# Kernel optimization log

Measured on AMD Instinct MI355X. Metric: run time of the kernel, lower is better.

## Reference

```python
import jax, jax.numpy as jnp
import numpy as np

B, N, G = 8, 512, 16          # images, proposals/img, gt boxes/img
C = 91                        # num classes (incl background)
FEAT = 256 * 7 * 7            # pooled RoI feature dim = 12544
REP = 1024                    # TwoMLPHead representation size
FG, BG = 0.5, 0.5             # fg/bg IoU thresholds
BBOX_W = (10.0, 10.0, 5.0, 5.0)
BETA = 1.0 / 9.0              # smooth-L1 beta


def setup_inputs() -> dict:
    key = jax.random.key(0)
    ks = jax.random.split(key, 12)
    # valid xyxy boxes inside an ~800x800 image
    tl = jax.random.uniform(ks[0], (B, N, 2), minval=0.0, maxval=700.0)
    wh = jax.random.uniform(ks[1], (B, N, 2), minval=8.0, maxval=128.0)
    proposals = jnp.concatenate([tl, tl + wh], axis=-1)
    gtl = jax.random.uniform(ks[2], (B, G, 2), minval=0.0, maxval=700.0)
    gwh = jax.random.uniform(ks[3], (B, G, 2), minval=8.0, maxval=128.0)
    gt_boxes = jnp.concatenate([gtl, gtl + gwh], axis=-1)
    gt_labels = jax.random.randint(ks[4], (B, G), 1, C)  # foreground labels 1..C-1
    P = N + G
    features = jax.random.normal(ks[5], (B * P, FEAT), dtype=jnp.float32)
    s = 0.01
    return {
        'proposals': proposals, 'gt_boxes': gt_boxes, 'features': features,
        'W1': jax.random.normal(ks[6], (FEAT, REP), jnp.float32) * s,
        'b1': jnp.zeros((REP,), jnp.float32),
        'W2': jax.random.normal(ks[7], (REP, REP), jnp.float32) * s,
        'b2': jnp.zeros((REP,), jnp.float32),
        'Wcls': jax.random.normal(ks[8], (REP, C), jnp.float32) * s,
        'bcls': jnp.zeros((C,), jnp.float32),
        'Wbox': jax.random.normal(ks[9], (REP, C * 4), jnp.float32) * s,
        'bbox': jnp.zeros((C * 4,), jnp.float32),
        'gt_labels': gt_labels,
    }


def _box_iou(gt, pr):
    # gt: [B,G,4], pr: [B,P,4] -> [B,G,P]
    area_g = (gt[..., 2] - gt[..., 0]) * (gt[..., 3] - gt[..., 1])
    area_p = (pr[..., 2] - pr[..., 0]) * (pr[..., 3] - pr[..., 1])
    lt = jnp.maximum(gt[:, :, None, :2], pr[:, None, :, :2])
    rb = jnp.minimum(gt[:, :, None, 2:], pr[:, None, :, 2:])
    wh = jnp.clip(rb - lt, 0.0)
    inter = wh[..., 0] * wh[..., 1]
    return inter / (area_g[:, :, None] + area_p[:, None, :] - inter)


def _encode(ref, gt):
    # torchvision BoxCoder.encode_single; ref/gt: [...,4]
    wx, wy, ww, wh = BBOX_W
    ew = ref[..., 2] - ref[..., 0]; eh = ref[..., 3] - ref[..., 1]
    ex = ref[..., 0] + 0.5 * ew;    ey = ref[..., 1] + 0.5 * eh
    gw = gt[..., 2] - gt[..., 0];   gh = gt[..., 3] - gt[..., 1]
    gx = gt[..., 0] + 0.5 * gw;     gy = gt[..., 1] + 0.5 * gh
    return jnp.stack([
        wx * (gx - ex) / ew, wy * (gy - ey) / eh,
        ww * jnp.log(gw / ew), wh * jnp.log(gh / eh)], axis=-1)


def reference(proposals, gt_boxes, features, W1, b1, W2, b2, Wcls, bcls, Wbox, bbox, gt_labels):
    # add_gt_proposals
    props = jnp.concatenate([proposals, gt_boxes], axis=1)  # [B,P,4]
    # assign_targets_to_proposals (Matcher, allow_low_quality_matches=False)
    iou = _box_iou(gt_boxes, props)                          # [B,G,P]
    matched_vals = iou.max(axis=1)                           # [B,P]
    matched_idx = iou.argmax(axis=1)                         # [B,P]
    labels = jnp.take_along_axis(gt_labels, matched_idx, axis=1)
    labels = jnp.where(matched_vals < BG, 0, labels)                         # background
    labels = jnp.where((matched_vals >= BG) & (matched_vals < FG), -1, labels)  # ignore
    matched_gt = jnp.take_along_axis(gt_boxes, matched_idx[..., None], axis=1)  # [B,P,4]
    reg_targets = _encode(props, matched_gt).reshape(-1, 4)  # [R,4]
    labels = labels.reshape(-1)                               # [R]

    # TwoMLPHead + FastRCNNPredictor
    x = jax.nn.relu(features @ W1 + b1)
    x = jax.nn.relu(x @ W2 + b2)
    class_logits = x @ Wcls + bcls                            # [R,C]
    box_regression = (x @ Wbox + bbox).reshape(-1, C, 4)      # [R,C,4]

    # fastrcnn_loss (all proposals; ignored labels (-1) masked from CE)
    R = class_logits.shape[0]
    valid = (labels >= 0).astype(class_logits.dtype)
    safe_lab = jnp.clip(labels, 0, C - 1)
    logp = jax.nn.log_softmax(class_logits, axis=-1)
    nll = -jnp.take_along_axis(logp, safe_lab[:, None], axis=1)[:, 0]
    classification_loss = (nll * valid).sum() / jnp.maximum(valid.sum(), 1.0)

    pos = (labels > 0).astype(class_logits.dtype)
    pred = jnp.take_along_axis(box_regression, safe_lab[:, None, None], axis=1)[:, 0]  # [R,4]
    d = jnp.abs(pred - reg_targets)
    sl1 = jnp.where(d < BETA, 0.5 * d * d / BETA, d - 0.5 * BETA).sum(-1)
    box_loss = (sl1 * pos).sum() / R

    return jnp.stack([classification_loss, box_loss])
```

## Files before the change

kernel.cpp:

```cpp
#include <hip/hip_runtime.h>
#include <cstdint>
#include <cstddef>

#define BQ   8
#define NP   512
#define GQ   16
#define PP   528
#define RT   4224
#define CC   91
#define FEATD 12544
#define REPD 1024
#define NH   512
#define NHU  455
#define BETA (1.0f/9.0f)
#define WSC  64.0f

typedef float f32x4 __attribute__((ext_vector_type(4)));
typedef int   v8i  __attribute__((ext_vector_type(8)));
typedef float v16f __attribute__((ext_vector_type(16)));

__device__ __forceinline__ unsigned short f2bf(float f) {
  unsigned int x = __float_as_uint(f);
  unsigned int r = (x + 0x7fffu + ((x >> 16) & 1u)) >> 16;
  return (unsigned short)r;
}
__device__ __forceinline__ float bf2f(unsigned short u) {
  return __uint_as_float((unsigned int)u << 16);
}

__device__ __forceinline__ void ld_lds16(const void* g, void* l) {
  __builtin_amdgcn_global_load_lds(
      (const __attribute__((address_space(1))) void*)g,
      (__attribute__((address_space(3))) void*)l, 16, 0, 0);
}

__device__ __forceinline__ size_t img_off(int row, int kb, int KT) {
  return (size_t)((row >> 7) * KT + (kb >> 6)) * 8192
       + (size_t)((((row >> 5) & 3) << 11) + (((kb >> 4) & 3) << 9)
                  + ((row & 31) << 4) + (kb & 15));
}

constexpr size_t O_W1T = 0;
constexpr size_t SZ_W1T = (size_t)FEATD * REPD;
constexpr size_t O_W2T = O_W1T + SZ_W1T;
constexpr size_t SZ_W2T = (size_t)REPD * REPD;
constexpr size_t O_WH  = O_W2T + SZ_W2T;
constexpr size_t SZ_WH = (size_t)NH * REPD;
constexpr size_t O_BH  = O_WH + SZ_WH;
constexpr size_t SZ_BH = (size_t)NH * 4;
constexpr size_t O_X1  = O_BH + SZ_BH;
constexpr size_t SZ_X1 = (size_t)RT * REPD;
constexpr size_t O_X2  = O_X1 + SZ_X1;
constexpr size_t O_LAB = O_X2 + SZ_X1;
constexpr size_t O_TGT = O_LAB + (size_t)RT * 4;
constexpr size_t O_NLL = O_TGT + (size_t)RT * 16;
constexpr size_t O_VC  = O_NLL + (size_t)RT * 4;
constexpr size_t O_SL1 = O_VC + (size_t)RT * 4;
constexpr size_t O_PART = ((O_SL1 + (size_t)RT * 4) + 255) & ~(size_t)255;
constexpr size_t SZ_PART = (size_t)4 * RT * REPD * 2;
constexpr size_t O_F8 = O_PART + SZ_PART;

#define NB_CV ((RT/128)*(FEATD/64))
__global__ void prep_cv(const float* __restrict__ feat, unsigned char* __restrict__ feat8) {
  int b = blockIdx.x, t = threadIdx.x;
  int yb = b / (FEATD / 64), kt = b % (FEATD / 64);
  const int w = t >> 6, L = t & 63;
  const int rl = L & 31, h = L >> 5;
  const float* src = feat + (size_t)(yb * 128 + w * 32 + rl) * FEATD + kt * 64 + h * 32;
  unsigned char* dst = feat8 + (size_t)b * 8192 + w * 2048 + rl * 16;
  unsigned int pk[8];
#pragma unroll
  for (int c = 0; c < 8; ++c) {
    float4 f = ((const float4*)src)[c];
    unsigned int r = (unsigned int)__builtin_amdgcn_cvt_pk_fp8_f32(f.x, f.y, 0, false);
    pk[c] = (unsigned int)__builtin_amdgcn_cvt_pk_fp8_f32(f.z, f.w, (int)r, true);
  }
  int4 v0; v0.x = (int)pk[0]; v0.y = (int)pk[1]; v0.z = (int)pk[2]; v0.w = (int)pk[3];
  int4 v1; v1.x = (int)pk[4]; v1.y = (int)pk[5]; v1.z = (int)pk[6]; v1.w = (int)pk[7];
  *(int4*)(dst + (2 * h) * 512) = v0;
  *(int4*)(dst + (2 * h + 1) * 512) = v1;
}

__device__ __forceinline__ void tr128(const float* __restrict__ in, unsigned char* __restrict__ out,
                                      int K, int N, int row_off, int KT,
                                      int bx, int by, int t, float (*tile)[36]) {
  const int n0 = bx * 32, k0 = by * 128;
  const int n4 = t & 7, kr = t >> 3;
  if (n0 + 32 <= N) {
#pragma unroll
    for (int i = 0; i < 4; ++i) {
      int k = k0 + kr + i * 32;
      float4 f = *(const float4*)&in[(size_t)k * N + n0 + n4 * 4];
      *(float4*)&tile[kr + i * 32][n4 * 4] = f;
    }
  } else {
#pragma unroll
    for (int i = 0; i < 4; ++i) {
      int k = k0 + kr + i * 32;
#pragma unroll
      for (int j = 0; j < 4; ++j) {
        int n = n0 + n4 * 4 + j;
        tile[kr + i * 32][n4 * 4 + j] = (n < N) ? in[(size_t)k * N + n] : 0.0f;
      }
    }
  }
  __syncthreads();
  const int rn = t & 31, kc = t >> 5;
  const int n = n0 + rn;
  if (n < N) {
    unsigned int pk[4];
#pragma unroll
    for (int q = 0; q < 4; ++q) {
      float f0 = tile[kc * 16 + q * 4 + 0][rn] * WSC;
      float f1 = tile[kc * 16 + q * 4 + 1][rn] * WSC;
      float f2 = tile[kc * 16 + q * 4 + 2][rn] * WSC;
      float f3 = tile[kc * 16 + q * 4 + 3][rn] * WSC;
      unsigned int r = (unsigned int)__builtin_amdgcn_cvt_pk_fp8_f32(f0, f1, 0, false);
      pk[q] = (unsigned int)__builtin_amdgcn_cvt_pk_fp8_f32(f2, f3, (int)r, true);
    }
    int4 v; v.x = (int)pk[0]; v.y = (int)pk[1]; v.z = (int)pk[2]; v.w = (int)pk[3];
    *(int4*)&out[img_off(n + row_off, k0 + kc * 16, KT)] = v;
  }
}

#define NBW1 ((REPD/32)*(FEATD/128))
#define NBW2 ((REPD/32)*(REPD/128))
#define NBWC (3*(REPD/128))
#define NBWB (12*(REPD/128))
#define NB_PW (NBW1+NBW2+NBWC+NBWB)

__global__ void prep_w(const float* __restrict__ W1, const float* __restrict__ W2,
                       const float* __restrict__ Wcls, const float* __restrict__ Wbox,
                       unsigned char* __restrict__ W1t, unsigned char* __restrict__ W2t,
                       unsigned char* __restrict__ Wh) {
  __shared__ float tile[128][36];
  int b = blockIdx.x, t = threadIdx.x;
  if (b < NBW1) { tr128(W1, W1t, FEATD, REPD, 0, FEATD/64, b % 32, b / 32, t, tile); return; }
  b -= NBW1;
  if (b < NBW2) { tr128(W2, W2t, REPD, REPD, 0, REPD/64, b % 32, b / 32, t, tile); return; }
  b -= NBW2;
  if (b < NBWC) { tr128(Wcls, Wh, REPD, CC, 0, REPD/64, b % 3, b / 3, t, tile); return; }
  b -= NBWC;
  tr128(Wbox, Wh, REPD, 4 * CC, CC, REPD/64, b % 12, b / 12, t, tile);
}

#define NB_HI 230
#define NB_MT 17
#define NB_MISC (NB_HI+NB_MT)
__global__ void prep_misc(const float* __restrict__ bcls, const float* __restrict__ bbox,
                          const float* __restrict__ proposals, const float* __restrict__ gt_boxes,
                          const int* __restrict__ gt_labels,
                          unsigned char* __restrict__ Wh, float* __restrict__ bh,
                          int* __restrict__ labels, float* __restrict__ tgts) {
  int b = blockIdx.x, t = threadIdx.x;
  if (b < NB_HI) {
    int idx = b * 256 + t;
    const int npad = (NH - NHU) * REPD;
    if (idx < npad) {
      int row = NHU + (idx >> 10), k = idx & 1023;
      Wh[img_off(row, k, REPD/64)] = 0;
    } else {
      int i2 = idx - npad;
      if (i2 < NH) bh[i2] = (i2 < CC) ? bcls[i2] : (i2 < NHU ? bbox[i2 - CC] : 0.0f);
    }
    return;
  }
  b -= NB_HI;
  int r = b * 256 + t;
  if (r >= RT) return;
  int bi_ = r / PP, p = r % PP;
  float x0, y0, x1, y1;
  if (p < NP) {
    const float* qq = proposals + ((size_t)bi_ * NP + p) * 4;
    x0 = qq[0]; y0 = qq[1]; x1 = qq[2]; y1 = qq[3];
  } else {
    const float* qq = gt_boxes + ((size_t)bi_ * GQ + (p - NP)) * 4;
    x0 = qq[0]; y0 = qq[1]; x1 = qq[2]; y1 = qq[3];
  }
  float ap = (x1 - x0) * (y1 - y0);
  float best = -1.0f; int bg = 0;
#pragma unroll
  for (int g = 0; g < GQ; ++g) {
    const float* gb = gt_boxes + ((size_t)bi_ * GQ + g) * 4;
    float gx0 = gb[0], gy0 = gb[1], gx1 = gb[2], gy1 = gb[3];
    float ag = (gx1 - gx0) * (gy1 - gy0);
    float iw = fmaxf(fminf(gx1, x1) - fmaxf(gx0, x0), 0.0f);
    float ih = fmaxf(fminf(gy1, y1) - fmaxf(gy0, y0), 0.0f);
    float inter = iw * ih;
    float iou = inter / (ag + ap - inter);
    if (iou > best) { best = iou; bg = g; }
  }
  int lab = gt_labels[bi_ * GQ + bg];
  if (best < 0.5f) lab = 0;
  labels[r] = lab;
  const float* gb = gt_boxes + ((size_t)bi_ * GQ + bg) * 4;
  float ew = x1 - x0, eh = y1 - y0;
  float ex = x0 + 0.5f * ew, ey = y0 + 0.5f * eh;
  float gw = gb[2] - gb[0], gh = gb[3] - gb[1];
  float gx = gb[0] + 0.5f * gw, gy = gb[1] + 0.5f * gh;
  tgts[r * 4 + 0] = 10.0f * (gx - ex) / ew;
  tgts[r * 4 + 1] = 10.0f * (gy - ey) / eh;
  tgts[r * 4 + 2] = 5.0f * logf(gw / ew);
  tgts[r * 4 + 3] = 5.0f * logf(gh / eh);
}

__global__ __launch_bounds__(256, 4)
void gemm_f8(const unsigned char* __restrict__ Aimg, const unsigned char* __restrict__ Bimg,
             unsigned short* __restrict__ P, int M, int Nc, int KT, int nkt,
             int n_nblk, int n_my, int npairs) {
  __shared__ unsigned char As[2 * 8192];
  __shared__ unsigned char Bs[2 * 8192];

  const int g = blockIdx.x;
  const int xcd = g & 7;
  const int kix = g >> 3;
  const int n  = kix % n_nblk;
  const int pi = kix / n_nblk;
  const int p  = pi * 8 + xcd;
  if (p >= npairs) return;
  const int y  = p % n_my;
  const int kz = p / n_my;
  const int m0 = y * 128, n0 = n * 128;

  const int tid = threadIdx.x;
  const int w = tid >> 6, L = tid & 63;
  const int l31 = L & 31, h = L >> 5;
  const int wr = (w >> 1) * 64, wc = (w & 1) * 64;

  const int kt0 = kz * nkt;
  const unsigned char* gA = Aimg + ((size_t)y * KT + kt0) * 8192 + w * 2048 + L * 16;
  const unsigned char* gB = Bimg + ((size_t)n * KT + kt0) * 8192 + w * 2048 + L * 16;
  const int lw = w * 2048;

#define STAGE(it, bufo) do {                                    \
    const size_t _go = (size_t)(it) * 8192;                     \
    ld_lds16(gA + _go,        &As[(bufo) + lw]);                \
    ld_lds16(gA + _go + 1024, &As[(bufo) + lw + 1024]);         \
    ld_lds16(gB + _go,        &Bs[(bufo) + lw]);                \
    ld_lds16(gB + _go + 1024, &Bs[(bufo) + lw + 1024]);         \
  } while (0)

  int aoff[2], boff[2];
#pragma unroll
  for (int i = 0; i < 2; ++i) {
    aoff[i] = (((w >> 1) * 2 + i) << 11) + (h << 10) + (l31 << 4);
    boff[i] = (((w & 1) * 2 + i) << 11) + (h << 10) + (l31 << 4);
  }

  STAGE(0, 0);

  v16f acc[2][2] = {};
  int cur = 0;
  for (int it = 0; it < nkt; ++it) {
    const int cb = cur << 13;
    if (it + 1 < nkt) {
      STAGE(it + 1, cb ^ 8192);
      asm volatile("s_waitcnt vmcnt(4)" ::: "memory");
    } else {
      asm volatile("s_waitcnt vmcnt(0)" ::: "memory");
    }
    __builtin_amdgcn_sched_barrier(0);
    __builtin_amdgcn_s_barrier();

    v8i a[2], b[2];
#pragma unroll
    for (int i = 0; i < 2; ++i) {
      int4 alo = *(const int4*)&As[cb + aoff[i]];
      int4 ahi = *(const int4*)&As[cb + aoff[i] + 512];
      a[i] = (v8i){alo.x, alo.y, alo.z, alo.w, ahi.x, ahi.y, ahi.z, ahi.w};
      int4 blo = *(const int4*)&Bs[cb + boff[i]];
      int4 bhi = *(const int4*)&Bs[cb + boff[i] + 512];
      b[i] = (v8i){blo.x, blo.y, blo.z, blo.w, bhi.x, bhi.y, bhi.z, bhi.w};
    }
#pragma unroll
    for (int i = 0; i < 2; ++i)
#pragma unroll
      for (int j = 0; j < 2; ++j)
        acc[i][j] = __builtin_amdgcn_mfma_scale_f32_32x32x64_f8f6f4(
            a[i], b[j], acc[i][j], 0, 0, 0, 127, 0, 127);

    asm volatile("s_waitcnt lgkmcnt(0)" ::: "memory");
    __builtin_amdgcn_sched_barrier(0);
    __builtin_amdgcn_s_barrier();
    cur ^= 1;
  }
#undef STAGE

  unsigned short* Pz = P + (size_t)kz * M * Nc;
#pragma unroll
  for (int i = 0; i < 2; ++i) {
#pragma unroll
    for (int j = 0; j < 2; ++j) {
      int colb = n0 + wc + j * 32 + l31;
#pragma unroll
      for (int r = 0; r < 16; ++r) {
        int row = m0 + wr + i * 32 + (r & 3) + 8 * (r >> 2) + 4 * h;
        Pz[(size_t)row * Nc + colb] = f2bf(acc[i][j][r]);
      }
    }
  }
}

template <int S>
__global__ void reduce_fp8k(const unsigned short* __restrict__ P, const float* __restrict__ bias,
                            unsigned int* __restrict__ outp, long MN4, int nc4) {
  long i = (long)blockIdx.x * blockDim.x + threadIdx.x;
  long stride = (long)gridDim.x * blockDim.x;
  const ushort4* P4 = (const ushort4*)P;
  const float4* B4 = (const float4*)bias;
  for (; i < MN4; i += stride) {
    float vx = 0, vy = 0, vz = 0, vw = 0;
#pragma unroll
    for (int s = 0; s < S; ++s) {
      ushort4 u = P4[s * MN4 + i];
      vx += bf2f(u.x); vy += bf2f(u.y); vz += bf2f(u.z); vw += bf2f(u.w);
    }
    float4 b = B4[i & (nc4 - 1)];
    vx = fmaxf(vx * (1.0f / WSC) + b.x, 0.0f);
    vy = fmaxf(vy * (1.0f / WSC) + b.y, 0.0f);
    vz = fmaxf(vz * (1.0f / WSC) + b.z, 0.0f);
    vw = fmaxf(vw * (1.0f / WSC) + b.w, 0.0f);
    unsigned int r = (unsigned int)__builtin_amdgcn_cvt_pk_fp8_f32(vx, vy, 0, false);
    r = (unsigned int)__builtin_amdgcn_cvt_pk_fp8_f32(vz, vw, (int)r, true);
    int rr = (int)(i >> 8);
    int kb = ((int)i & 255) * 4;
    outp[img_off(rr, kb, REPD / 64) >> 2] = r;
  }
}

__global__ void loss_row(const unsigned short* __restrict__ P, const float* __restrict__ bh,
                         const int* __restrict__ labels, const float* __restrict__ tgts,
                         float* __restrict__ nll_v, float* __restrict__ vc_v,
                         float* __restrict__ sl1_v) {
  int r = blockIdx.x;
  int l = threadIdx.x;
  const size_t SL = (size_t)RT * NH;
  const unsigned short* p0 = P + (size_t)r * NH;
#define COLV(c) ((bf2f(p0[(c)]) + bf2f(p0[SL + (c)]) + bf2f(p0[2 * SL + (c)]) + \
                  bf2f(p0[3 * SL + (c)])) * (1.0f / WSC) + bh[(c)])
  float v1 = COLV(l);
  float v2 = (l < CC - 64) ? COLV(64 + l) : -3.4e38f;
  float m = fmaxf(v1, v2);
#pragma unroll
  for (int o = 32; o; o >>= 1) m = fmaxf(m, __shfl_xor(m, o));
  float e = __expf(v1 - m) + ((l < CC - 64) ? __expf(v2 - m) : 0.0f);
#pragma unroll
  for (int o = 32; o; o >>= 1) e += __shfl_xor(e, o);
  if (l == 0) {
    float lse = m + __logf(e);
    int lab = labels[r];
    int sl = lab < 0 ? 0 : (lab > CC - 1 ? CC - 1 : lab);
    float valid = (lab >= 0) ? 1.0f : 0.0f;
    nll_v[r] = (lse - COLV(sl)) * valid;
    vc_v[r] = valid;
    float s = 0.0f;
#pragma unroll
    for (int d = 0; d < 4; ++d) {
      float pd = COLV(CC + sl * 4 + d);
      float ad = fabsf(pd - tgts[r * 4 + d]);
      s += (ad < BETA) ? 0.5f * ad * ad / BETA : ad - 0.5f * BETA;
    }
    sl1_v[r] = (lab > 0) ? s : 0.0f;
  }
#undef COLV
}

__global__ void reduce_final(const float* __restrict__ nll_v, const float* __restrict__ vc_v,
                             const float* __restrict__ sl1_v, float* __restrict__ out) {
  __shared__ float s1[256], s2[256], s3[256];
  int t = threadIdx.x;
  float a = 0, b = 0, c = 0;
  for (int i = t; i < RT; i += 256) { a += nll_v[i]; b += vc_v[i]; c += sl1_v[i]; }
  s1[t] = a; s2[t] = b; s3[t] = c;
  __syncthreads();
  for (int o = 128; o; o >>= 1) {
    if (t < o) { s1[t] += s1[t + o]; s2[t] += s2[t + o]; s3[t] += s3[t + o]; }
    __syncthreads();
  }
  if (t == 0) {
    out[0] = s1[0] / fmaxf(s2[0], 1.0f);
    out[1] = s3[0] / (float)RT;
  }
}

extern "C" void kernel_launch(void* const* d_in, const int* in_sizes, int n_in,
                              void* d_out, int out_size, void* d_ws, size_t ws_size,
                              hipStream_t stream) {
  const float* proposals = (const float*)d_in[0];
  const float* gt_boxes  = (const float*)d_in[1];
  const float* features  = (const float*)d_in[2];
  const float* W1   = (const float*)d_in[3];
  const float* b1   = (const float*)d_in[4];
  const float* W2   = (const float*)d_in[5];
  const float* b2   = (const float*)d_in[6];
  const float* Wcls = (const float*)d_in[7];
  const float* bcls = (const float*)d_in[8];
  const float* Wbox = (const float*)d_in[9];
  const float* bbox = (const float*)d_in[10];
  const int* gt_labels = (const int*)d_in[11];
  float* out = (float*)d_out;

  char* ws = (char*)d_ws;
  unsigned char* W1t = (unsigned char*)(ws + O_W1T);
  unsigned char* W2t = (unsigned char*)(ws + O_W2T);
  unsigned char* Wh  = (unsigned char*)(ws + O_WH);
  float* bh          = (float*)(ws + O_BH);
  unsigned char* x1  = (unsigned char*)(ws + O_X1);
  unsigned char* x2  = (unsigned char*)(ws + O_X2);
  int* labels        = (int*)(ws + O_LAB);
  float* tgts        = (float*)(ws + O_TGT);
  float* nll_v       = (float*)(ws + O_NLL);
  float* vc_v        = (float*)(ws + O_VC);
  float* sl1_v       = (float*)(ws + O_SL1);
  unsigned short* part = (unsigned short*)(ws + O_PART);
  unsigned char* feat8 = (unsigned char*)(ws + O_F8);

  prep_cv<<<NB_CV, 256, 0, stream>>>(features, feat8);
  prep_w<<<NB_PW, 256, 0, stream>>>(W1, W2, Wcls, Wbox, W1t, W2t, Wh);
  prep_misc<<<NB_MISC, 256, 0, stream>>>(bcls, bbox, proposals, gt_boxes, gt_labels,
                                         Wh, bh, labels, tgts);

  gemm_f8<<<1088, 256, 0, stream>>>(feat8, W1t, part, RT, REPD, FEATD/64, 49,
                                    8, 33, 132);
  reduce_fp8k<4><<<2048, 256, 0, stream>>>(part, b1, (unsigned int*)x1,
                                           (long)RT * REPD / 4, REPD / 4);

  gemm_f8<<<576, 256, 0, stream>>>(x1, W2t, part, RT, REPD, REPD/64, 8,
                                   8, 33, 66);
  reduce_fp8k<2><<<2048, 256, 0, stream>>>(part, b2, (unsigned int*)x2,
                                           (long)RT * REPD / 4, REPD / 4);

  gemm_f8<<<544, 256, 0, stream>>>(x2, Wh, part, RT, NH, REPD/64, 4,
                                   4, 33, 132);

  loss_row<<<RT, 64, 0, stream>>>(part, bh, labels, tgts, nll_v, vc_v, sl1_v);
  reduce_final<<<1, 256, 0, stream>>>(nll_v, vc_v, sl1_v, out);
}
```

Measured before the change: 482.1 us.

## Enlarge FP8 GEMM tiles to 256x256 with 512-thread blocks and padded M

```diff
diff --git a/kernel.cpp b/kernel.cpp
--- a/kernel.cpp
+++ b/kernel.cpp
@@ -7,6 +7,7 @@
 #define GQ   16
 #define PP   528
 #define RT   4224
+#define MPAD 4352
 #define CC   91
 #define FEATD 12544
 #define REPD 1024
@@ -49,7 +50,7 @@
 constexpr size_t O_BH  = O_WH + SZ_WH;
 constexpr size_t SZ_BH = (size_t)NH * 4;
 constexpr size_t O_X1  = O_BH + SZ_BH;
-constexpr size_t SZ_X1 = (size_t)RT * REPD;
+constexpr size_t SZ_X1 = (size_t)MPAD * REPD;
 constexpr size_t O_X2  = O_X1 + SZ_X1;
 constexpr size_t O_LAB = O_X2 + SZ_X1;
 constexpr size_t O_TGT = O_LAB + (size_t)RT * 4;
@@ -57,17 +58,24 @@
 constexpr size_t O_VC  = O_NLL + (size_t)RT * 4;
 constexpr size_t O_SL1 = O_VC + (size_t)RT * 4;
 constexpr size_t O_PART = ((O_SL1 + (size_t)RT * 4) + 255) & ~(size_t)255;
-constexpr size_t SZ_PART = (size_t)4 * RT * REPD * 2;
+constexpr size_t SZ_PART = (size_t)4 * MPAD * REPD * 2;
 constexpr size_t O_F8 = O_PART + SZ_PART;
 
-#define NB_CV ((RT/128)*(FEATD/64))
+#define NKT1 (FEATD/64)
+#define NB_CV ((MPAD/128)*NKT1)
 __global__ void prep_cv(const float* __restrict__ feat, unsigned char* __restrict__ feat8) {
   int b = blockIdx.x, t = threadIdx.x;
-  int yb = b / (FEATD / 64), kt = b % (FEATD / 64);
+  int yb = b / NKT1, kt = b % NKT1;
   const int w = t >> 6, L = t & 63;
   const int rl = L & 31, h = L >> 5;
+  unsigned char* dst = feat8 + (size_t)b * 8192 + w * 2048 + rl * 16;
+  if (yb == 33) {
+    int4 z; z.x = z.y = z.z = z.w = 0;
+    *(int4*)(dst + (2 * h) * 512) = z;
+    *(int4*)(dst + (2 * h + 1) * 512) = z;
+    return;
+  }
   const float* src = feat + (size_t)(yb * 128 + w * 32 + rl) * FEATD + kt * 64 + h * 32;
-  unsigned char* dst = feat8 + (size_t)b * 8192 + w * 2048 + rl * 16;
   unsigned int pk[8];
 #pragma unroll
   for (int c = 0; c < 8; ++c) {
@@ -204,12 +212,12 @@
   tgts[r * 4 + 3] = 5.0f * logf(gh / eh);
 }
 
-__global__ __launch_bounds__(256, 4)
+__global__ __launch_bounds__(512, 4)
 void gemm_f8(const unsigned char* __restrict__ Aimg, const unsigned char* __restrict__ Bimg,
-             unsigned short* __restrict__ P, int M, int Nc, int KT, int nkt,
+             unsigned short* __restrict__ P, int Mp, int Nc, int KT, int nkt,
              int n_nblk, int n_my, int npairs) {
-  __shared__ unsigned char As[2 * 8192];
-  __shared__ unsigned char Bs[2 * 8192];
+  __shared__ unsigned char As[2 * 16384];
+  __shared__ unsigned char Bs[2 * 16384];
 
   const int g = blockIdx.x;
   const int xcd = g & 7;
@@ -220,16 +228,17 @@
   if (p >= npairs) return;
   const int y  = p % n_my;
   const int kz = p / n_my;
-  const int m0 = y * 128, n0 = n * 128;
+  const int m0 = y * 256, n0 = n * 256;
 
   const int tid = threadIdx.x;
   const int w = tid >> 6, L = tid & 63;
   const int l31 = L & 31, h = L >> 5;
-  const int wr = (w >> 1) * 64, wc = (w & 1) * 64;
 
   const int kt0 = kz * nkt;
-  const unsigned char* gA = Aimg + ((size_t)y * KT + kt0) * 8192 + w * 2048 + L * 16;
-  const unsigned char* gB = Bimg + ((size_t)n * KT + kt0) * 8192 + w * 2048 + L * 16;
+  const unsigned char* gA = Aimg + ((size_t)((2 * y + (w >> 2)) * KT + kt0)) * 8192
+                                 + (w & 3) * 2048 + L * 16;
+  const unsigned char* gB = Bimg + ((size_t)((2 * n + (w >> 2)) * KT + kt0)) * 8192
+                                 + (w & 3) * 2048 + L * 16;
   const int lw = w * 2048;
 
 #define STAGE(it, bufo) do {                                    \
@@ -240,21 +249,22 @@
     ld_lds16(gB + _go + 1024, &Bs[(bufo) + lw + 1024]);         \
   } while (0)
 
-  int aoff[2], boff[2];
-#pragma unroll
-  for (int i = 0; i < 2; ++i) {
-    aoff[i] = (((w >> 1) * 2 + i) << 11) + (h << 10) + (l31 << 4);
-    boff[i] = (((w & 1) * 2 + i) << 11) + (h << 10) + (l31 << 4);
-  }
+  int aoff[4], boff[2];
+#pragma unroll
+  for (int i = 0; i < 4; ++i)
+    aoff[i] = (((w >> 2) * 4 + i) << 11) + (h << 10) + (l31 << 4);
+#pragma unroll
+  for (int j = 0; j < 2; ++j)
+    boff[j] = (((w & 3) * 2 + j) << 11) + (h << 10) + (l31 << 4);
 
   STAGE(0, 0);
 
-  v16f acc[2][2] = {};
+  v16f acc[4][2] = {};
   int cur = 0;
   for (int it = 0; it < nkt; ++it) {
-    const int cb = cur << 13;
+    const int cb = cur << 14;
     if (it + 1 < nkt) {
-      STAGE(it + 1, cb ^ 8192);
+      STAGE(it + 1, cb ^ 16384);
       asm volatile("s_waitcnt vmcnt(4)" ::: "memory");
     } else {
       asm volatile("s_waitcnt vmcnt(0)" ::: "memory");
@@ -262,18 +272,21 @@
     __builtin_amdgcn_sched_barrier(0);
     __builtin_amdgcn_s_barrier();
 
-    v8i a[2], b[2];
-#pragma unroll
-    for (int i = 0; i < 2; ++i) {
+    v8i a[4], b[2];
+#pragma unroll
+    for (int i = 0; i < 4; ++i) {
       int4 alo = *(const int4*)&As[cb + aoff[i]];
       int4 ahi = *(const int4*)&As[cb + aoff[i] + 512];
       a[i] = (v8i){alo.x, alo.y, alo.z, alo.w, ahi.x, ahi.y, ahi.z, ahi.w};
-      int4 blo = *(const int4*)&Bs[cb + boff[i]];
-      int4 bhi = *(const int4*)&Bs[cb + boff[i] + 512];
-      b[i] = (v8i){blo.x, blo.y, blo.z, blo.w, bhi.x, bhi.y, bhi.z, bhi.w};
-    }
-#pragma unroll
-    for (int i = 0; i < 2; ++i)
+    }
+#pragma unroll
+    for (int j = 0; j < 2; ++j) {
+      int4 blo = *(const int4*)&Bs[cb + boff[j]];
+      int4 bhi = *(const int4*)&Bs[cb + boff[j] + 512];
+      b[j] = (v8i){blo.x, blo.y, blo.z, blo.w, bhi.x, bhi.y, bhi.z, bhi.w};
+    }
+#pragma unroll
+    for (int i = 0; i < 4; ++i)
 #pragma unroll
       for (int j = 0; j < 2; ++j)
         acc[i][j] = __builtin_amdgcn_mfma_scale_f32_32x32x64_f8f6f4(
@@ -286,15 +299,15 @@
   }
 #undef STAGE
 
-  unsigned short* Pz = P + (size_t)kz * M * Nc;
-#pragma unroll
-  for (int i = 0; i < 2; ++i) {
+  unsigned short* Pz = P + (size_t)kz * Mp * Nc;
+#pragma unroll
+  for (int i = 0; i < 4; ++i) {
 #pragma unroll
     for (int j = 0; j < 2; ++j) {
-      int colb = n0 + wc + j * 32 + l31;
+      int colb = n0 + (w & 3) * 64 + j * 32 + l31;
 #pragma unroll
       for (int r = 0; r < 16; ++r) {
-        int row = m0 + wr + i * 32 + (r & 3) + 8 * (r >> 2) + 4 * h;
+        int row = m0 + (w >> 2) * 128 + i * 32 + (r & 3) + 8 * (r >> 2) + 4 * h;
         Pz[(size_t)row * Nc + colb] = f2bf(acc[i][j][r]);
       }
     }
@@ -303,7 +316,7 @@
 
 template <int S>
 __global__ void reduce_fp8k(const unsigned short* __restrict__ P, const float* __restrict__ bias,
-                            unsigned int* __restrict__ outp, long MN4, int nc4) {
+                            unsigned int* __restrict__ outp, long MN4, long slice4, int nc4) {
   long i = (long)blockIdx.x * blockDim.x + threadIdx.x;
   long stride = (long)gridDim.x * blockDim.x;
   const ushort4* P4 = (const ushort4*)P;
@@ -312,7 +325,7 @@
     float vx = 0, vy = 0, vz = 0, vw = 0;
 #pragma unroll
     for (int s = 0; s < S; ++s) {
-      ushort4 u = P4[s * MN4 + i];
+      ushort4 u = P4[s * slice4 + i];
       vx += bf2f(u.x); vy += bf2f(u.y); vz += bf2f(u.z); vw += bf2f(u.w);
     }
     float4 b = B4[i & (nc4 - 1)];
@@ -334,7 +347,7 @@
                          float* __restrict__ sl1_v) {
   int r = blockIdx.x;
   int l = threadIdx.x;
-  const size_t SL = (size_t)RT * NH;
+  const size_t SL = (size_t)MPAD * NH;
   const unsigned short* p0 = P + (size_t)r * NH;
 #define COLV(c) ((bf2f(p0[(c)]) + bf2f(p0[SL + (c)]) + bf2f(p0[2 * SL + (c)]) + \
                   bf2f(p0[3 * SL + (c)])) * (1.0f / WSC) + bh[(c)])
@@ -420,18 +433,20 @@
   prep_misc<<<NB_MISC, 256, 0, stream>>>(bcls, bbox, proposals, gt_boxes, gt_labels,
                                          Wh, bh, labels, tgts);
 
-  gemm_f8<<<1088, 256, 0, stream>>>(feat8, W1t, part, RT, REPD, FEATD/64, 49,
-                                    8, 33, 132);
+  gemm_f8<<<288, 512, 0, stream>>>(feat8, W1t, part, MPAD, REPD, FEATD/64, 49,
+                                   4, 17, 68);
   reduce_fp8k<4><<<2048, 256, 0, stream>>>(part, b1, (unsigned int*)x1,
-                                           (long)RT * REPD / 4, REPD / 4);
-
-  gemm_f8<<<576, 256, 0, stream>>>(x1, W2t, part, RT, REPD, REPD/64, 8,
-                                   8, 33, 66);
+                                           (long)RT * REPD / 4, (long)MPAD * REPD / 4,
+                                           REPD / 4);
+
+  gemm_f8<<<160, 512, 0, stream>>>(x1, W2t, part, MPAD, REPD, REPD/64, 8,
+                                   4, 17, 34);
   reduce_fp8k<2><<<2048, 256, 0, stream>>>(part, b2, (unsigned int*)x2,
-                                           (long)RT * REPD / 4, REPD / 4);
-
-  gemm_f8<<<544, 256, 0, stream>>>(x2, Wh, part, RT, NH, REPD/64, 4,
-                                   4, 33, 132);
+                                           (long)RT * REPD / 4, (long)MPAD * REPD / 4,
+                                           REPD / 4);
+
+  gemm_f8<<<144, 512, 0, stream>>>(x2, Wh, part, MPAD, NH, REPD/64, 4,
+                                   2, 17, 68);
 
   loss_row<<<RT, 64, 0, stream>>>(part, bh, labels, tgts, nll_v, vc_v, sl1_v);
   reduce_final<<<1, 256, 0, stream>>>(nll_v, vc_v, sl1_v, out);
```

Measured after the change: 1.153 ms. 2.39x slower.
